# Performance work log

Measured on AMD Instinct MI355X. Metric: run time of the kernel, lower is better.

## Reference

```python
import jax, jax.numpy as jnp
import numpy as np

MARGIN = 1.0


def setup_inputs() -> dict:
    key = jax.random.key(0)
    k1, k2, k3 = jax.random.split(key, 3)
    B, D, C = 16384, 256, 2000
    pred_embedding = jax.random.normal(k1, (B, D), dtype=jnp.float32)
    batch_label = jax.random.randint(k2, (B,), 0, C, dtype=jnp.int64)
    train_classes = jnp.arange(C, dtype=jnp.int64)
    train_sig = jax.random.normal(k3, (D, C), dtype=jnp.float32)
    return {
        "pred_embedding": pred_embedding,
        "batch_label": batch_label,
        "train_classes": train_classes,
        "train_sig": train_sig,
    }


def reference(pred_embedding, batch_label, train_classes, train_sig):
    # scores[j, k] = <pred_embedding[j], train_sig[:, train_classes[k]]>
    # Single GEMM replaces the per-pair dot-product loops.
    sig_cols = train_sig[:, train_classes]            # [D, C]
    scores = jnp.einsum("bd,dc->bc", pred_embedding, sig_cols)  # [B, C]
    # ground-truth class score per row: <XW_j, train_sig[:, y_j]>
    gt = jnp.einsum("bd,db->b", pred_embedding, train_sig[:, batch_label])  # [B]
    # exclude the class equal to the row label
    mask = (train_classes[None, :] != batch_label[:, None])  # [B, C] bool
    hinge = jnp.maximum(MARGIN + scores - gt[:, None], 0.0)
    loss = jnp.sum(jnp.where(mask, hinge, 0.0))
    return loss
```

## Files before the change

### kernel.cpp

```cpp
#include <hip/hip_runtime.h>

#define B_SZ 16384
#define D_SZ 256
#define C_SZ 2000
#define MARGIN_F 1.0f
#define NBLK 1024

typedef float floatx16 __attribute__((ext_vector_type(16)));

__device__ inline void gld_lds16(const void* g, void* l) {
  __builtin_amdgcn_global_load_lds(
      (const __attribute__((address_space(1))) void*)g,
      (__attribute__((address_space(3))) void*)l, 16, 0, 0);
}


__device__ inline int2 pack8_fp8(const float* v) {
  int lo = __builtin_amdgcn_cvt_pk_fp8_f32(v[0], v[1], 0, false);
  lo = __builtin_amdgcn_cvt_pk_fp8_f32(v[2], v[3], lo, true);
  int hi = __builtin_amdgcn_cvt_pk_fp8_f32(v[4], v[5], 0, false);
  hi = __builtin_amdgcn_cvt_pk_fp8_f32(v[6], v[7], hi, true);
  return make_int2(lo, hi);
}
__device__ inline float rt_fp8(float x) {
  int p = __builtin_amdgcn_cvt_pk_fp8_f32(x, x, 0, false);
  return __builtin_amdgcn_cvt_f32_fp8(p, 0);
}

__global__ __launch_bounds__(256) void prep_kernel(
    const float* __restrict__ pred, const float* __restrict__ sig,
    const int* __restrict__ label, char* __restrict__ predq,
    char* __restrict__ sigq, float* __restrict__ gt,
    float* __restrict__ out) {
  int bid = (int)blockIdx.x;
  int tid = threadIdx.x;

  if (tid < 64) {
    int t = bid * 64 + tid;
    if (t == 0) out[0] = 0.f;
    int ln = tid;
    int ks = (t >> 6) & 15, ct = t >> 10;
    int col = ct * 32 + (ln & 31);
    int kb = ks * 16 + (ln >> 5) * 8;
    float v[8];
#pragma unroll
    for (int j = 0; j < 8; j++)
      v[j] = (col < C_SZ) ? sig[(size_t)(kb + j) * C_SZ + col] : 0.f;
    *(int2*)(sigq + (size_t)t * 8) = pack8_fp8(v);
  }

  {
    int ri = tid & 15;
    int ks = tid >> 4;
    int tile = bid >> 1;
    int rhi = (bid & 1) * 16;
    const float4* p = (const float4*)(pred + (size_t)(bid * 16 + ri) * D_SZ + ks * 16);
    float4 f0 = p[0], f1 = p[1], f2 = p[2], f3 = p[3];
    float lo[8] = {f0.x, f0.y, f0.z, f0.w, f1.x, f1.y, f1.z, f1.w};
    float hi[8] = {f2.x, f2.y, f2.z, f2.w, f3.x, f3.y, f3.z, f3.w};
    size_t cbase = ((size_t)(tile * 16 + ks) * 64 + rhi + ri) * 8;
    *(int2*)(predq + cbase)          = pack8_fp8(lo);
    *(int2*)(predq + cbase + 32 * 8) = pack8_fp8(hi);
  }

  {
    int lane = tid & 63;
    int w = tid >> 6;
    int l = lane & 31;
    int half = lane >> 5;
#pragma unroll
    for (int it = 0; it < 2; it++) {
      int r = w * 4 + it * 2 + half;
      int row = bid * 16 + r;
      int lbl = label[row];
      const float* scol = sig + lbl;
      const float4* pr = (const float4*)(pred + (size_t)row * D_SZ + l * 8);
      float4 a0 = pr[0], a1 = pr[1];
      float pv[8] = {a0.x, a0.y, a0.z, a0.w, a1.x, a1.y, a1.z, a1.w};
      float s = 0.f;
#pragma unroll
      for (int j = 0; j < 8; j++) {
        float sv = rt_fp8(scol[(size_t)(l * 8 + j) * C_SZ]);
        s += rt_fp8(pv[j]) * sv;
      }
#pragma unroll
      for (int off = 16; off > 0; off >>= 1) s += __shfl_down(s, off, 32);
      if (l == 0) gt[row] = s;
    }
  }
}

__global__ __launch_bounds__(256) void mfma_fused_kernel(
    const char* __restrict__ predq, const char* __restrict__ sigq,
    const float* __restrict__ gt, float* __restrict__ out) {
  __shared__ char Bs[4096 * 8];
  __shared__ float gtl[256];
  __shared__ float red[4];
  int tid = threadIdx.x;
  int lane = tid & 63;
  int w = tid >> 6;
  int kh = lane >> 5, lm = lane & 31;
  int bid = (int)blockIdx.x;
  int i = bid >> 3;
  int rsb = (bid & 7) * 8 + (i & 7);
  int cg = i >> 3;

#pragma unroll
  for (int s = 0; s < 8; s++) {
    int q0 = s * 256 + w * 64;
    gld_lds16(sigq + ((size_t)cg * 2048 + q0 + lane) * 16, (void*)(Bs + (size_t)q0 * 16));
  }
  if (w == 0)
    gld_lds16((const char*)gt + (size_t)rsb * 1024 + (size_t)lane * 16, (void*)gtl);

  const char* abase0 = predq + (size_t)(rsb * 8 + w * 2) * 8192 + (size_t)lane * 8;
  long afr[16];
#pragma unroll
  for (int ks = 0; ks < 16; ks++)
    afr[ks] = *(const long*)(abase0 + (size_t)ks * 512);
  __syncthreads();

  float sum = 0.f;
#pragma unroll
  for (int rt = 0; rt < 2; rt++) {
    if (rt == 1) {
      const char* abase1 = abase0 + 8192;
#pragma unroll
      for (int ks = 0; ks < 16; ks++)
        afr[ks] = *(const long*)(abase1 + (size_t)ks * 512);
    }
#pragma unroll
    for (int ct = 0; ct < 4; ct++) {
      floatx16 acc = {};
      const char* bbase = Bs + (size_t)ct * 8192 + (size_t)lane * 8;
#pragma unroll
      for (int ks = 0; ks < 16; ks++) {
        long b = *(const long*)(bbase + (size_t)ks * 512);
        acc = __builtin_amdgcn_mfma_f32_32x32x16_fp8_fp8(afr[ks], b, acc, 0, 0, 0);
      }
      int col = cg * 128 + ct * 32 + lm;
      float keep = (col < C_SZ) ? 1.f : 0.f;
#pragma unroll
      for (int reg = 0; reg < 16; reg++) {
        int rl = (reg & 3) + 8 * (reg >> 2) + 4 * kh;
        float mg = MARGIN_F - gtl[w * 64 + rt * 32 + rl];
        sum += keep * fmaxf(acc[reg] + mg, 0.f);
      }
    }
  }
#pragma unroll
  for (int off = 32; off > 0; off >>= 1) sum += __shfl_down(sum, off, 64);
  if (lane == 0) red[w] = sum;
  __syncthreads();
  if (tid == 0)
    atomicAdd(out, red[0] + red[1] + red[2] + red[3]
                   - (float)B_SZ * MARGIN_F / (float)NBLK);
}

extern "C" void kernel_launch(void* const* d_in, const int* in_sizes, int n_in,
                              void* d_out, int out_size, void* d_ws, size_t ws_size,
                              hipStream_t stream) {
  const float* pred  = (const float*)d_in[0];
  const int*   label = (const int*)d_in[1];
  const float* sig   = (const float*)d_in[3];
  float* out = (float*)d_out;

  float* gt    = (float*)d_ws;
  char*  predq = (char*)d_ws + (128 << 10);
  char*  sigq  = (char*)d_ws + (128 << 10) + (4 << 20);

  prep_kernel<<<1024, 256, 0, stream>>>(pred, sig, label, predq, sigq, gt, out);
  mfma_fused_kernel<<<NBLK, 256, 0, stream>>>(predq, sigq, gt, out);
}
```

Before: 107.2 us.

## Compute ground-truth scores inside the fused MFMA kernel from quantized data

Moves the per-row ground-truth dot product out of the prep kernel and into the fused GEMM kernel, which now writes it straight into shared memory. It reads the already-quantized fp8 pred and sig buffers instead of gathering fp32 sig columns with large strides. The aim is to drop the uncoalesced fp32 column gather and the global gt round trip. In exchange, each row's gt is recomputed by all 16 column-group blocks, and a serial 32-iteration shuffle loop now runs before the MFMA work in every block.

```diff
diff --git a/kernel.cpp b/kernel.cpp
--- a/kernel.cpp
+++ b/kernel.cpp
@@ -22,15 +22,16 @@
   hi = __builtin_amdgcn_cvt_pk_fp8_f32(v[6], v[7], hi, true);
   return make_int2(lo, hi);
 }
-__device__ inline float rt_fp8(float x) {
-  int p = __builtin_amdgcn_cvt_pk_fp8_f32(x, x, 0, false);
-  return __builtin_amdgcn_cvt_f32_fp8(p, 0);
+__device__ inline void unpack4_fp8(int w, float* o) {
+  o[0] = __builtin_amdgcn_cvt_f32_fp8(w, 0);
+  o[1] = __builtin_amdgcn_cvt_f32_fp8(w, 1);
+  o[2] = __builtin_amdgcn_cvt_f32_fp8(w, 2);
+  o[3] = __builtin_amdgcn_cvt_f32_fp8(w, 3);
 }
 
-__global__ __launch_bounds__(256) void prep_kernel(
+__global__ __launch_bounds__(256) void quant_kernel(
     const float* __restrict__ pred, const float* __restrict__ sig,
-    const int* __restrict__ label, char* __restrict__ predq,
-    char* __restrict__ sigq, float* __restrict__ gt,
+    char* __restrict__ predq, char* __restrict__ sigq,
     float* __restrict__ out) {
   int bid = (int)blockIdx.x;
   int tid = threadIdx.x;
@@ -62,37 +63,11 @@
     *(int2*)(predq + cbase)          = pack8_fp8(lo);
     *(int2*)(predq + cbase + 32 * 8) = pack8_fp8(hi);
   }
-
-  {
-    int lane = tid & 63;
-    int w = tid >> 6;
-    int l = lane & 31;
-    int half = lane >> 5;
-#pragma unroll
-    for (int it = 0; it < 2; it++) {
-      int r = w * 4 + it * 2 + half;
-      int row = bid * 16 + r;
-      int lbl = label[row];
-      const float* scol = sig + lbl;
-      const float4* pr = (const float4*)(pred + (size_t)row * D_SZ + l * 8);
-      float4 a0 = pr[0], a1 = pr[1];
-      float pv[8] = {a0.x, a0.y, a0.z, a0.w, a1.x, a1.y, a1.z, a1.w};
-      float s = 0.f;
-#pragma unroll
-      for (int j = 0; j < 8; j++) {
-        float sv = rt_fp8(scol[(size_t)(l * 8 + j) * C_SZ]);
-        s += rt_fp8(pv[j]) * sv;
-      }
-#pragma unroll
-      for (int off = 16; off > 0; off >>= 1) s += __shfl_down(s, off, 32);
-      if (l == 0) gt[row] = s;
-    }
-  }
 }
 
 __global__ __launch_bounds__(256) void mfma_fused_kernel(
     const char* __restrict__ predq, const char* __restrict__ sigq,
-    const float* __restrict__ gt, float* __restrict__ out) {
+    const int* __restrict__ label, float* __restrict__ out) {
   __shared__ char Bs[4096 * 8];
   __shared__ float gtl[256];
   __shared__ float red[4];
@@ -110,8 +85,32 @@
     int q0 = s * 256 + w * 64;
     gld_lds16(sigq + ((size_t)cg * 2048 + q0 + lane) * 16, (void*)(Bs + (size_t)q0 * 16));
   }
-  if (w == 0)
-    gld_lds16((const char*)gt + (size_t)rsb * 1024 + (size_t)lane * 16, (void*)gtl);
+
+  {
+    int l = lane & 31;
+    int half = lane >> 5;
+    int rq0 = w * 2 + half;
+    int lblv = label[rsb * 256 + l * 8 + rq0];
+#pragma unroll 4
+    for (int it = 0; it < 32; ++it) {
+      int q = it * 8 + rq0;
+      int lbl = __shfl(lblv, it, 32);
+      int tile = rsb * 8 + (q >> 5), r31 = q & 31;
+      int2 pv8 = *(const int2*)(predq +
+          (((size_t)(tile * 16 + (l >> 1)) * 64) + (l & 1) * 32 + r31) * 8);
+      int2 sv8 = *(const int2*)(sigq +
+          (((size_t)((lbl >> 5) * 16 + (l >> 1)) * 64) + (l & 1) * 32 + (lbl & 31)) * 8);
+      float pv[8], sv[8];
+      unpack4_fp8(pv8.x, pv); unpack4_fp8(pv8.y, pv + 4);
+      unpack4_fp8(sv8.x, sv); unpack4_fp8(sv8.y, sv + 4);
+      float s = 0.f;
+#pragma unroll
+      for (int j = 0; j < 8; j++) s += pv[j] * sv[j];
+#pragma unroll
+      for (int off = 16; off > 0; off >>= 1) s += __shfl_down(s, off, 32);
+      if (l == 0) gtl[q] = s;
+    }
+  }
 
   const char* abase0 = predq + (size_t)(rsb * 8 + w * 2) * 8192 + (size_t)lane * 8;
   long afr[16];
@@ -165,10 +164,9 @@
   const float* sig   = (const float*)d_in[3];
   float* out = (float*)d_out;
 
-  float* gt    = (float*)d_ws;
-  char*  predq = (char*)d_ws + (128 << 10);
-  char*  sigq  = (char*)d_ws + (128 << 10) + (4 << 20);
+  char* predq = (char*)d_ws + (128 << 10);
+  char* sigq  = (char*)d_ws + (128 << 10) + (4 << 20);
 
-  prep_kernel<<<1024, 256, 0, stream>>>(pred, sig, label, predq, sigq, gt, out);
-  mfma_fused_kernel<<<NBLK, 256, 0, stream>>>(predq, sigq, gt, out);
+  quant_kernel<<<1024, 256, 0, stream>>>(pred, sig, predq, sigq, out);
+  mfma_fused_kernel<<<NBLK, 256, 0, stream>>>(predq, sigq, label, out);
 }
```

Result: slower. 121.5 us (+13.4%).
